# Optimization experiments

Hardware: AMD Instinct MI355X
Metric: run time of the kernel (lower is better)

Reference implementation:

```python
import jax, jax.numpy as jnp
import numpy as np

D, E, FF = 512, 8, 4 * 512
BS, H, W = 2, 32, 32
T = BS * H * W


def setup_inputs() -> dict:
    key = jax.random.key(0)
    ks = jax.random.split(key, 12)
    s = lambda fan_in: 1.0 / np.sqrt(fan_in)
    return {
        "x": jax.random.normal(ks[0], (BS, D, H, W), dtype=jnp.float32),
        "Wg": jax.random.normal(ks[1], (D, E), dtype=jnp.float32) * s(D),
        "bg": jnp.zeros((E,), dtype=jnp.float32),
        "Wn": jax.random.normal(ks[2], (D, E), dtype=jnp.float32) * s(D),
        "bn": jnp.zeros((E,), dtype=jnp.float32),
        "W1": jax.random.normal(ks[3], (E, D, FF), dtype=jnp.float32) * s(D),
        "b1": jnp.zeros((E, FF), dtype=jnp.float32),
        "W2": jax.random.normal(ks[4], (E, FF, D), dtype=jnp.float32) * s(FF),
        "b2": jnp.zeros((E, D), dtype=jnp.float32),
        "noise_eps": jax.random.normal(ks[5], (T, E), dtype=jnp.float32),
        "top_k": 2,
    }


def reference(x, Wg, bg, Wn, bn, W1, b1, W2, b2, noise_eps, top_k):
    bs, d, h, w = x.shape
    tokens = x.transpose(0, 2, 3, 1).reshape(-1, d)  # [T, d]
    t = tokens.shape[0]
    # Noisy top-k router
    logits = tokens @ Wg + bg                                  # [T, E]
    noise = noise_eps * jax.nn.softplus(tokens @ Wn + bn)      # [T, E]
    noisy = logits + noise
    top_v, top_i = jax.lax.top_k(noisy, top_k)                 # [T, k]
    sparse = jnp.full_like(noisy, -jnp.inf)
    sparse = sparse.at[jnp.arange(t)[:, None], top_i].set(top_v)
    gates = jax.nn.softmax(sparse, axis=-1)                    # [T, E], zero off top-k
    # Expert MLPs (dense over experts; gates zero-out non-selected)
    hdn = jax.nn.relu(jnp.einsum("td,edf->tef", tokens, W1) + b1)  # [T, E, 4d]
    out_e = jnp.einsum("tef,efd->ted", hdn, W2) + b2               # [T, E, d]
    out = jnp.einsum("te,ted->td", gates, out_e)                   # combine
    return out.reshape(bs, h, w, d).transpose(0, 3, 1, 2)
```

## Files before the change

### kernel.cpp

```cpp
#include <hip/hip_runtime.h>
#include <hip/hip_bf16.h>
#include <math.h>

#define DD  512
#define EE  8
#define FFD 2048
#define TT  2048
#define HWH 1024

typedef __bf16 b16x8 __attribute__((ext_vector_type(8)));
typedef float  f32x4 __attribute__((ext_vector_type(4)));

__device__ __forceinline__ unsigned short f2bf(float f) {
    unsigned u = __builtin_bit_cast(unsigned, f);
    u = (u + 0x7FFFu + ((u >> 16) & 1u)) >> 16;
    return (unsigned short)u;
}

__device__ __forceinline__ void gload16(const void* g, void* l) {
    __builtin_amdgcn_global_load_lds(
        (const __attribute__((address_space(1))) void*)g,
        (__attribute__((address_space(3))) void*)l, 16, 0, 0);
}

__device__ __forceinline__ int seg_pred(const int* __restrict__ cnt, int e) {
    int s = 0;
    #pragma unroll
    for (int i = 0; i < EE; ++i) s += (i < e) ? cnt[i] : 0;
    return s;
}

__global__ __launch_bounds__(256) void moe_prep(
    const float* __restrict__ W1, const float* __restrict__ W2,
    const float* __restrict__ x,
    unsigned short* __restrict__ W1t, unsigned short* __restrict__ W2t,
    unsigned short* __restrict__ xb,
    const float* __restrict__ Wg, const float* __restrict__ Wn,
    float* __restrict__ part, int* __restrict__ cnt)
{
    __shared__ float ld[128][65];
    int which = blockIdx.z, e = blockIdx.y;
    int tid = threadIdx.x;

    if (which == 3) {
        if (e == 0 && blockIdx.x == 0 && tid < EE) cnt[tid] = 0;
        if (blockIdx.x >= 32) return;
        int u = tid & 63;
        int q = tid >> 6;
        int tt = blockIdx.x, dc = e;
        int t = tt * 64 + u;
        int b = t >> 10, hw = t & 1023;
        const float* xp = x + (size_t)b * DD * HWH + hw;
        int d0 = dc * 64 + q * 16;
        float accL[EE], accN[EE];
        #pragma unroll
        for (int k = 0; k < EE; ++k) { accL[k] = 0.f; accN[k] = 0.f; }
        #pragma unroll
        for (int i = 0; i < 16; ++i) {
            int d = d0 + i;
            float tv = xp[(size_t)d * HWH];
            #pragma unroll
            for (int k = 0; k < EE; ++k) {
                accL[k] = fmaf(tv, Wg[d * EE + k], accL[k]);
                accN[k] = fmaf(tv, Wn[d * EE + k], accN[k]);
            }
        }
        float (*s)[64][16] = (float (*)[64][16])&ld[0][0];
        #pragma unroll
        for (int k = 0; k < EE; ++k) { s[q][u][k] = accL[k]; s[q][u][k + 8] = accN[k]; }
        __syncthreads();
        int idx = tid * 4;
        int ot = idx >> 4, oc = idx & 15;
        float4 v;
        v.x = s[0][ot][oc+0] + s[1][ot][oc+0] + s[2][ot][oc+0] + s[3][ot][oc+0];
        v.y = s[0][ot][oc+1] + s[1][ot][oc+1] + s[2][ot][oc+1] + s[3][ot][oc+1];
        v.z = s[0][ot][oc+2] + s[1][ot][oc+2] + s[2][ot][oc+2] + s[3][ot][oc+2];
        v.w = s[0][ot][oc+3] + s[1][ot][oc+3] + s[2][ot][oc+3] + s[3][ot][oc+3];
        *(float4*)&part[((size_t)dc * TT + tt * 64 + ot) * 16 + oc] = v;
        return;
    }

    const float* in; unsigned short* out; int R, C;
    if (which == 0)      { R = DD;  C = FFD; in = W1 + (size_t)e*DD*FFD; out = W1t + (size_t)e*FFD*DD; }
    else if (which == 1) { R = FFD; C = DD;  in = W2 + (size_t)e*FFD*DD; out = W2t + (size_t)e*DD*FFD; }
    else { if (e >= 2) return; R = DD; C = HWH; in = x + (size_t)e*DD*HWH; out = xb + (size_t)e*HWH*DD; }
    int tilesC = C >> 6, tilesR = R >> 7;
    if ((int)blockIdx.x >= tilesR * tilesC) return;
    int tr = (blockIdx.x / tilesC) << 7, tc = (blockIdx.x % tilesC) << 6;
    int ty = tid >> 4, tx = tid & 15;
    #pragma unroll
    for (int i = 0; i < 8; ++i) {
        int r = ty + i * 16;
        const float4 v = *(const float4*)&in[(size_t)(tr + r)*C + tc + tx*4];
        ld[r][tx*4+0] = v.x; ld[r][tx*4+1] = v.y;
        ld[r][tx*4+2] = v.z; ld[r][tx*4+3] = v.w;
    }
    __syncthreads();
    int ox = tid & 15;
    #pragma unroll
    for (int it = 0; it < 4; ++it) {
        int c = (tid >> 4) + it * 16;
        uint4 u;
        u.x = f2bf(ld[ox*8+0][c]) | ((unsigned)f2bf(ld[ox*8+1][c]) << 16);
        u.y = f2bf(ld[ox*8+2][c]) | ((unsigned)f2bf(ld[ox*8+3][c]) << 16);
        u.z = f2bf(ld[ox*8+4][c]) | ((unsigned)f2bf(ld[ox*8+5][c]) << 16);
        u.w = f2bf(ld[ox*8+6][c]) | ((unsigned)f2bf(ld[ox*8+7][c]) << 16);
        *(uint4*)&out[(size_t)(tc + c)*R + tr + ox*8] = u;
    }
}

__global__ __launch_bounds__(256) void moe_router_topk(
    const float* __restrict__ part,
    const float* __restrict__ bg, const float* __restrict__ bn,
    const float* __restrict__ neps,
    int* __restrict__ cnt, int* __restrict__ pair0, int* __restrict__ pair1,
    int* __restrict__ ltok, float* __restrict__ lgate)
{
    int t = blockIdx.x * 256 + threadIdx.x;
    float L[EE], N[EE];
    #pragma unroll
    for (int e = 0; e < EE; ++e) { L[e] = bg[e]; N[e] = bn[e]; }
    #pragma unroll
    for (int dc = 0; dc < 8; ++dc) {
        const float* p = &part[((size_t)dc * TT + t) * 16];
        float4 a0 = *(const float4*)&p[0];
        float4 a1 = *(const float4*)&p[4];
        float4 a2 = *(const float4*)&p[8];
        float4 a3 = *(const float4*)&p[12];
        L[0] += a0.x; L[1] += a0.y; L[2] += a0.z; L[3] += a0.w;
        L[4] += a1.x; L[5] += a1.y; L[6] += a1.z; L[7] += a1.w;
        N[0] += a2.x; N[1] += a2.y; N[2] += a2.z; N[3] += a2.w;
        N[4] += a3.x; N[5] += a3.y; N[6] += a3.z; N[7] += a3.w;
    }
    float noisy[EE];
    #pragma unroll
    for (int e = 0; e < EE; ++e) {
        float sp = fmaxf(N[e], 0.f) + log1pf(expf(-fabsf(N[e])));
        noisy[e] = L[e] + neps[t * EE + e] * sp;
    }
    int e0 = 0; float v0 = noisy[0];
    #pragma unroll
    for (int e = 1; e < EE; ++e) if (noisy[e] > v0) { v0 = noisy[e]; e0 = e; }
    int e1 = (e0 == 0) ? 1 : 0; float v1 = noisy[e1];
    #pragma unroll
    for (int e = 0; e < EE; ++e)
        if (e != e0 && e != e1 && noisy[e] > v1) { v1 = noisy[e]; e1 = e; }
    float ex  = expf(v1 - v0);
    float inv = 1.f / (1.f + ex);
    float g0 = inv, g1 = ex * inv;
    int p0 = atomicAdd(&cnt[e0], 1);
    int p1 = atomicAdd(&cnt[e1], 1);
    ltok[e0 * TT + p0] = t; lgate[e0 * TT + p0] = g0;
    ltok[e1 * TT + p1] = t; lgate[e1 * TT + p1] = g1;
    pair0[t] = (e0 << 16) | p0;
    pair1[t] = (e1 << 16) | p1;
}

__global__ __launch_bounds__(256, 3) void moe_gemm1(
    const unsigned short* __restrict__ xb, const unsigned short* __restrict__ W1t,
    const float* __restrict__ b1, const int* __restrict__ cnt,
    const int* __restrict__ ltok, unsigned short* __restrict__ Hbuf)
{
    int e = blockIdx.x, mt = blockIdx.y, nt = blockIdx.z;
    int ce = cnt[e];
    if (mt * 64 >= ce) return;
    int s0 = seg_pred(cnt, e);
    const unsigned short* Be = W1t + (size_t)e * FFD * DD;
    __shared__ unsigned short As[2][64 * 64];
    __shared__ unsigned short Bs[2][128 * 64];
    int tid = threadIdx.x, lane = tid & 63, wv = tid >> 6;

    int srow = lane >> 3, schunk = lane & 7;
    int srcoff = ((schunk ^ srow) << 3);

    size_t aoff[2]; int ards[2];
    #pragma unroll
    for (int c = 0; c < 2; ++c) {
        int r0 = (c*4 + wv)*8;
        int ri = mt*64 + r0 + srow;
        int tok = ltok[e * TT + (ri < ce ? ri : 0)];
        aoff[c] = (size_t)tok * DD + srcoff;
        ards[c] = r0 * 64;
    }
    size_t boff[4]; int brds[4];
    #pragma unroll
    for (int c = 0; c < 4; ++c) {
        int r0 = (c*4 + wv)*8;
        boff[c] = (size_t)(nt*128 + r0 + srow) * DD + srcoff;
        brds[c] = r0 * 64;
    }

    int frow = lane & 15, fk = (lane >> 4) * 8;
    int am = (wv >> 1) * 32, bnn = (wv & 1) * 64;
    int rx = (frow & 7) << 3;

    f32x4 acc[2][4];
    f32x4 zero = {0.f, 0.f, 0.f, 0.f};
    #pragma unroll
    for (int m = 0; m < 2; ++m)
        #pragma unroll
        for (int n = 0; n < 4; ++n) acc[m][n] = zero;

    #pragma unroll
    for (int c = 0; c < 2; ++c) gload16(&xb[aoff[c]], &As[0][ards[c]]);
    #pragma unroll
    for (int c = 0; c < 4; ++c) gload16(&Be[boff[c]], &Bs[0][brds[c]]);
    #pragma unroll
    for (int c = 0; c < 2; ++c) gload16(&xb[aoff[c] + 64], &As[1][ards[c]]);
    #pragma unroll
    for (int c = 0; c < 4; ++c) gload16(&Be[boff[c] + 64], &Bs[1][brds[c]]);

    #pragma unroll
    for (int t = 0; t < 8; ++t) {
        if (t < 6) { asm volatile("s_waitcnt vmcnt(6)" ::: "memory"); }
        else       { asm volatile("s_waitcnt vmcnt(0)" ::: "memory"); }
        __builtin_amdgcn_s_barrier();
        __builtin_amdgcn_sched_barrier(0);
        const int cur = t & 1;
        #pragma unroll
        for (int k2 = 0; k2 < 64; k2 += 32) {
            b16x8 af[2], bf[4];
            #pragma unroll
            for (int m = 0; m < 2; ++m)
                af[m] = *(const b16x8*)&As[cur][(am + m*16 + frow)*64 + ((k2 + fk) ^ rx)];
            #pragma unroll
            for (int n = 0; n < 4; ++n)
                bf[n] = *(const b16x8*)&Bs[cur][(bnn + n*16 + frow)*64 + ((k2 + fk) ^ rx)];
            #pragma unroll
            for (int m = 0; m < 2; ++m)
                #pragma unroll
                for (int n = 0; n < 4; ++n)
                    acc[m][n] = __builtin_amdgcn_mfma_f32_16x16x32_bf16(af[m], bf[n], acc[m][n], 0, 0, 0);
        }
        __builtin_amdgcn_s_barrier();
        if (t < 6) {
            int kk = (t + 2) * 64;
            #pragma unroll
            for (int c = 0; c < 2; ++c) gload16(&xb[aoff[c] + kk], &As[cur][ards[c]]);
            #pragma unroll
            for (int c = 0; c < 4; ++c) gload16(&Be[boff[c] + kk], &Bs[cur][brds[c]]);
        }
    }

    int crow = (lane >> 4) * 4;
    #pragma unroll
    for (int m = 0; m < 2; ++m) {
        #pragma unroll
        for (int i = 0; i < 4; ++i) {
            int r = mt*64 + am + m*16 + crow + i;
            if (r < ce) {
                size_t hrow = (size_t)(s0 + r) * FFD;
                #pragma unroll
                for (int n = 0; n < 4; ++n) {
                    int col = nt*128 + bnn + n*16 + frow;
                    float v = acc[m][n][i] + b1[e * FFD + col];
                    Hbuf[hrow + col] = f2bf(fmaxf(v, 0.f));
                }
            }
        }
    }
}

__global__ __launch_bounds__(256, 3) void moe_gemm2(
    const unsigned short* __restrict__ Hbuf, const unsigned short* __restrict__ W2t,
    const int* __restrict__ cnt, float* __restrict__ P2)
{
    int e = blockIdx.x, mt = blockIdx.y;
    int split = blockIdx.z >> 2, nt = blockIdx.z & 3;
    int ce = cnt[e];
    if (mt * 64 >= ce) return;
    int s0 = seg_pred(cnt, e);
    int kbase = split * 1024;
    const unsigned short* Be = W2t + (size_t)e * DD * FFD;
    __shared__ unsigned short As[2][64 * 64];
    __shared__ unsigned short Bs[2][128 * 64];
    int tid = threadIdx.x, lane = tid & 63, wv = tid >> 6;

    int srow = lane >> 3, schunk = lane & 7;
    int srcoff = ((schunk ^ srow) << 3);

    size_t aoff[2]; int ards[2];
    #pragma unroll
    for (int c = 0; c < 2; ++c) {
        int r0 = (c*4 + wv)*8;
        int g = s0 + mt*64 + r0 + srow; if (g > 4095) g = 4095;
        aoff[c] = (size_t)g * FFD + kbase + srcoff;
        ards[c] = r0 * 64;
    }
    size_t boff[4]; int brds[4];
    #pragma unroll
    for (int c = 0; c < 4; ++c) {
        int r0 = (c*4 + wv)*8;
        boff[c] = (size_t)(nt*128 + r0 + srow) * FFD + kbase + srcoff;
        brds[c] = r0 * 64;
    }

    int frow = lane & 15, fk = (lane >> 4) * 8;
    int am = (wv >> 1) * 32, bnn = (wv & 1) * 64;
    int rx = (frow & 7) << 3;

    f32x4 acc[2][4];
    f32x4 zero = {0.f, 0.f, 0.f, 0.f};
    #pragma unroll
    for (int m = 0; m < 2; ++m)
        #pragma unroll
        for (int n = 0; n < 4; ++n) acc[m][n] = zero;

    #pragma unroll
    for (int c = 0; c < 2; ++c) gload16(&Hbuf[aoff[c]], &As[0][ards[c]]);
    #pragma unroll
    for (int c = 0; c < 4; ++c) gload16(&Be[boff[c]], &Bs[0][brds[c]]);
    #pragma unroll
    for (int c = 0; c < 2; ++c) gload16(&Hbuf[aoff[c] + 64], &As[1][ards[c]]);
    #pragma unroll
    for (int c = 0; c < 4; ++c) gload16(&Be[boff[c] + 64], &Bs[1][brds[c]]);

    #pragma unroll
    for (int t = 0; t < 16; ++t) {
        if (t < 14) { asm volatile("s_waitcnt vmcnt(6)" ::: "memory"); }
        else        { asm volatile("s_waitcnt vmcnt(0)" ::: "memory"); }
        __builtin_amdgcn_s_barrier();
        __builtin_amdgcn_sched_barrier(0);
        const int cur = t & 1;
        #pragma unroll
        for (int k2 = 0; k2 < 64; k2 += 32) {
            b16x8 af[2], bf[4];
            #pragma unroll
            for (int m = 0; m < 2; ++m)
                af[m] = *(const b16x8*)&As[cur][(am + m*16 + frow)*64 + ((k2 + fk) ^ rx)];
            #pragma unroll
            for (int n = 0; n < 4; ++n)
                bf[n] = *(const b16x8*)&Bs[cur][(bnn + n*16 + frow)*64 + ((k2 + fk) ^ rx)];
            #pragma unroll
            for (int m = 0; m < 2; ++m)
                #pragma unroll
                for (int n = 0; n < 4; ++n)
                    acc[m][n] = __builtin_amdgcn_mfma_f32_16x16x32_bf16(af[m], bf[n], acc[m][n], 0, 0, 0);
        }
        __builtin_amdgcn_s_barrier();
        if (t < 14) {
            int kk = (t + 2) * 64;
            #pragma unroll
            for (int c = 0; c < 2; ++c) gload16(&Hbuf[aoff[c] + kk], &As[cur][ards[c]]);
            #pragma unroll
            for (int c = 0; c < 4; ++c) gload16(&Be[boff[c] + kk], &Bs[cur][brds[c]]);
        }
    }

    int crow = (lane >> 4) * 4;
    float* Pw = P2 + (size_t)split * 4096 * DD;
    #pragma unroll
    for (int m = 0; m < 2; ++m) {
        #pragma unroll
        for (int i = 0; i < 4; ++i) {
            int r = mt*64 + am + m*16 + crow + i;
            if (r < ce) {
                size_t prow = (size_t)(s0 + r) * DD;
                #pragma unroll
                for (int n = 0; n < 4; ++n) {
                    int col = nt*128 + bnn + n*16 + frow;
                    Pw[prow + col] = acc[m][n][i];
                }
            }
        }
    }
}

__global__ __launch_bounds__(256) void moe_combine(
    const int* __restrict__ pair0, const int* __restrict__ pair1,
    const int* __restrict__ cnt, const float* __restrict__ lgate,
    const float* __restrict__ b2, const float* __restrict__ P2,
    float* __restrict__ out)
{
    __shared__ float tile[32][68];
    int tid = threadIdx.x;
    int ti = blockIdx.x, dc = blockIdx.y;
    int ty = tid >> 3, tx = tid & 7;
    int t = ti * 32 + ty;
    int a0 = pair0[t], a1 = pair1[t];
    int e0 = a0 >> 16, sl0 = a0 & 0xFFFF;
    int e1 = a1 >> 16, sl1 = a1 & 0xFFFF;
    int p0 = seg_pred(cnt, e0) + sl0, p1 = seg_pred(cnt, e1) + sl1;
    float g0 = lgate[e0 * TT + sl0], g1 = lgate[e1 * TT + sl1];
    int d0 = dc * 64 + tx * 8;
    f32x4 s0v[2] = {{0,0,0,0},{0,0,0,0}}, s1v[2] = {{0,0,0,0},{0,0,0,0}};
    #pragma unroll
    for (int s = 0; s < 2; ++s) {
        const f32x4* r0p = (const f32x4*)(P2 + ((size_t)s * 4096 + p0) * DD + d0);
        const f32x4* r1p = (const f32x4*)(P2 + ((size_t)s * 4096 + p1) * DD + d0);
        s0v[0] += r0p[0]; s0v[1] += r0p[1];
        s1v[0] += r1p[0]; s1v[1] += r1p[1];
    }
    const f32x4* b0p = (const f32x4*)(b2 + e0 * DD + d0);
    const f32x4* b1p = (const f32x4*)(b2 + e1 * DD + d0);
    #pragma unroll
    for (int q = 0; q < 2; ++q) {
        f32x4 v = g0 * (s0v[q] + b0p[q]) + g1 * (s1v[q] + b1p[q]);
        *(f32x4*)&tile[ty][tx*8 + q*4] = v;
    }
    __syncthreads();
    int dy = tid >> 2, hx = tid & 3;
    int b = (ti * 32) >> 10, hw0 = (ti * 32) & 1023;
    size_t obase = ((size_t)(b * DD + dc * 64 + dy)) * HWH + hw0;
    #pragma unroll
    for (int q = 0; q < 2; ++q) {
        int j = hx * 8 + q * 4;
        float4 w;
        w.x = tile[j + 0][dy];
        w.y = tile[j + 1][dy];
        w.z = tile[j + 2][dy];
        w.w = tile[j + 3][dy];
        *(float4*)&out[obase + j] = w;
    }
}

extern "C" void kernel_launch(void* const* d_in, const int* in_sizes, int n_in,
                              void* d_out, int out_size, void* d_ws, size_t ws_size,
                              hipStream_t stream)
{
    const float* x    = (const float*)d_in[0];
    const float* Wg   = (const float*)d_in[1];
    const float* bg   = (const float*)d_in[2];
    const float* Wn   = (const float*)d_in[3];
    const float* bn   = (const float*)d_in[4];
    const float* W1   = (const float*)d_in[5];
    const float* b1   = (const float*)d_in[6];
    const float* W2   = (const float*)d_in[7];
    const float* b2   = (const float*)d_in[8];
    const float* neps = (const float*)d_in[9];

    char* ws = (char*)d_ws;
    int*   cnt   = (int*)(ws + 0);
    int*   pair0 = (int*)(ws + 512);
    int*   pair1 = (int*)(ws + 8704);
    int*   ltok  = (int*)(ws + 32768);
    float* lgate = (float*)(ws + 98304);
    float* part  = (float*)(ws + 163840);
    unsigned short* xb   = (unsigned short*)(ws + 1212416);
    unsigned short* Hbuf = (unsigned short*)(ws + 3309568);
    unsigned short* W1t  = (unsigned short*)(ws + 20086784);
    unsigned short* W2t  = (unsigned short*)(ws + 36864000);
    float*          P2   = (float*)(ws + 53641216);

    moe_prep<<<dim3(128, 8, 4), 256, 0, stream>>>(W1, W2, x, W1t, W2t, xb, Wg, Wn, part, cnt);
    moe_router_topk<<<TT / 256, 256, 0, stream>>>(part, bg, bn, neps,
                                                  cnt, pair0, pair1, ltok, lgate);
    moe_gemm1<<<dim3(EE, 32, 16), 256, 0, stream>>>(xb, W1t, b1, cnt, ltok, Hbuf);
    moe_gemm2<<<dim3(EE, 32, 8), 256, 0, stream>>>(Hbuf, W2t, cnt, P2);
    moe_combine<<<dim3(TT / 32, 8), 256, 0, stream>>>(pair0, pair1, cnt, lgate, b2, P2, (float*)d_out);
}
```

Measured before the change: 91.42 us.

## Load A operand fragments directly from global into registers, drop A LDS tile

Both expert GEMM kernels now fetch their activation (A) fragments straight from global memory into double-buffered registers in MFMA fragment layout, instead of staging them through shared memory. The B tile stays in LDS. This frees LDS and removes A-side LDS writes and reads, and the launch bounds are raised from 3 to 4 blocks per CU. In exchange the A loads are narrower per-thread global reads with poorer coalescing, some rows are fetched redundantly by two waves, and register pressure rises. The vmcnt wait thresholds are retuned to account for the extra in-flight loads.

Measured after the change: 134.8 us. +47.4%, slower.

```diff
diff --git a/kernel.cpp b/kernel.cpp
--- a/kernel.cpp
+++ b/kernel.cpp
@@ -156,7 +156,7 @@
     pair1[t] = (e1 << 16) | p1;
 }
 
-__global__ __launch_bounds__(256, 3) void moe_gemm1(
+__global__ __launch_bounds__(256, 4) void moe_gemm1(
     const unsigned short* __restrict__ xb, const unsigned short* __restrict__ W1t,
     const float* __restrict__ b1, const int* __restrict__ cnt,
     const int* __restrict__ ltok, unsigned short* __restrict__ Hbuf)
@@ -166,22 +166,11 @@
     if (mt * 64 >= ce) return;
     int s0 = seg_pred(cnt, e);
     const unsigned short* Be = W1t + (size_t)e * FFD * DD;
-    __shared__ unsigned short As[2][64 * 64];
     __shared__ unsigned short Bs[2][128 * 64];
     int tid = threadIdx.x, lane = tid & 63, wv = tid >> 6;
 
     int srow = lane >> 3, schunk = lane & 7;
     int srcoff = ((schunk ^ srow) << 3);
-
-    size_t aoff[2]; int ards[2];
-    #pragma unroll
-    for (int c = 0; c < 2; ++c) {
-        int r0 = (c*4 + wv)*8;
-        int ri = mt*64 + r0 + srow;
-        int tok = ltok[e * TT + (ri < ce ? ri : 0)];
-        aoff[c] = (size_t)tok * DD + srcoff;
-        ards[c] = r0 * 64;
-    }
     size_t boff[4]; int brds[4];
     #pragma unroll
     for (int c = 0; c < 4; ++c) {
@@ -194,6 +183,10 @@
     int am = (wv >> 1) * 32, bnn = (wv & 1) * 64;
     int rx = (frow & 7) << 3;
 
+    int r0 = mt*64 + am + frow, r1 = r0 + 16;
+    const unsigned short* ap0 = xb + (size_t)ltok[e*TT + (r0 < ce ? r0 : 0)] * DD + fk;
+    const unsigned short* ap1 = xb + (size_t)ltok[e*TT + (r1 < ce ? r1 : 0)] * DD + fk;
+
     f32x4 acc[2][4];
     f32x4 zero = {0.f, 0.f, 0.f, 0.f};
     #pragma unroll
@@ -201,28 +194,31 @@
         #pragma unroll
         for (int n = 0; n < 4; ++n) acc[m][n] = zero;
 
-    #pragma unroll
-    for (int c = 0; c < 2; ++c) gload16(&xb[aoff[c]], &As[0][ards[c]]);
+    b16x8 ra[2][2][2];
+
     #pragma unroll
     for (int c = 0; c < 4; ++c) gload16(&Be[boff[c]], &Bs[0][brds[c]]);
-    #pragma unroll
-    for (int c = 0; c < 2; ++c) gload16(&xb[aoff[c] + 64], &As[1][ards[c]]);
+    __builtin_amdgcn_sched_barrier(0);
+    ra[0][0][0] = *(const b16x8*)&ap0[0];  ra[0][0][1] = *(const b16x8*)&ap0[32];
+    ra[0][1][0] = *(const b16x8*)&ap1[0];  ra[0][1][1] = *(const b16x8*)&ap1[32];
+    __builtin_amdgcn_sched_barrier(0);
     #pragma unroll
     for (int c = 0; c < 4; ++c) gload16(&Be[boff[c] + 64], &Bs[1][brds[c]]);
+    __builtin_amdgcn_sched_barrier(0);
+    ra[1][0][0] = *(const b16x8*)&ap0[64]; ra[1][0][1] = *(const b16x8*)&ap0[96];
+    ra[1][1][0] = *(const b16x8*)&ap1[64]; ra[1][1][1] = *(const b16x8*)&ap1[96];
+    __builtin_amdgcn_sched_barrier(0);
 
     #pragma unroll
     for (int t = 0; t < 8; ++t) {
-        if (t < 6) { asm volatile("s_waitcnt vmcnt(6)" ::: "memory"); }
+        if (t < 7) { asm volatile("s_waitcnt vmcnt(8)" ::: "memory"); }
         else       { asm volatile("s_waitcnt vmcnt(0)" ::: "memory"); }
         __builtin_amdgcn_s_barrier();
         __builtin_amdgcn_sched_barrier(0);
         const int cur = t & 1;
         #pragma unroll
         for (int k2 = 0; k2 < 64; k2 += 32) {
-            b16x8 af[2], bf[4];
-            #pragma unroll
-            for (int m = 0; m < 2; ++m)
-                af[m] = *(const b16x8*)&As[cur][(am + m*16 + frow)*64 + ((k2 + fk) ^ rx)];
+            b16x8 bf[4];
             #pragma unroll
             for (int n = 0; n < 4; ++n)
                 bf[n] = *(const b16x8*)&Bs[cur][(bnn + n*16 + frow)*64 + ((k2 + fk) ^ rx)];
@@ -230,15 +226,17 @@
             for (int m = 0; m < 2; ++m)
                 #pragma unroll
                 for (int n = 0; n < 4; ++n)
-                    acc[m][n] = __builtin_amdgcn_mfma_f32_16x16x32_bf16(af[m], bf[n], acc[m][n], 0, 0, 0);
+                    acc[m][n] = __builtin_amdgcn_mfma_f32_16x16x32_bf16(ra[cur][m][k2 >> 5], bf[n], acc[m][n], 0, 0, 0);
         }
         __builtin_amdgcn_s_barrier();
         if (t < 6) {
             int kk = (t + 2) * 64;
             #pragma unroll
-            for (int c = 0; c < 2; ++c) gload16(&xb[aoff[c] + kk], &As[cur][ards[c]]);
-            #pragma unroll
             for (int c = 0; c < 4; ++c) gload16(&Be[boff[c] + kk], &Bs[cur][brds[c]]);
+            __builtin_amdgcn_sched_barrier(0);
+            ra[cur][0][0] = *(const b16x8*)&ap0[kk];      ra[cur][0][1] = *(const b16x8*)&ap0[kk + 32];
+            ra[cur][1][0] = *(const b16x8*)&ap1[kk];      ra[cur][1][1] = *(const b16x8*)&ap1[kk + 32];
+            __builtin_amdgcn_sched_barrier(0);
         }
     }
 
@@ -261,7 +259,7 @@
     }
 }
 
-__global__ __launch_bounds__(256, 3) void moe_gemm2(
+__global__ __launch_bounds__(256, 4) void moe_gemm2(
     const unsigned short* __restrict__ Hbuf, const unsigned short* __restrict__ W2t,
     const int* __restrict__ cnt, float* __restrict__ P2)
 {
@@ -272,21 +270,11 @@
     int s0 = seg_pred(cnt, e);
     int kbase = split * 1024;
     const unsigned short* Be = W2t + (size_t)e * DD * FFD;
-    __shared__ unsigned short As[2][64 * 64];
     __shared__ unsigned short Bs[2][128 * 64];
     int tid = threadIdx.x, lane = tid & 63, wv = tid >> 6;
 
     int srow = lane >> 3, schunk = lane & 7;
     int srcoff = ((schunk ^ srow) << 3);
-
-    size_t aoff[2]; int ards[2];
-    #pragma unroll
-    for (int c = 0; c < 2; ++c) {
-        int r0 = (c*4 + wv)*8;
-        int g = s0 + mt*64 + r0 + srow; if (g > 4095) g = 4095;
-        aoff[c] = (size_t)g * FFD + kbase + srcoff;
-        ards[c] = r0 * 64;
-    }
     size_t boff[4]; int brds[4];
     #pragma unroll
     for (int c = 0; c < 4; ++c) {
@@ -299,6 +287,11 @@
     int am = (wv >> 1) * 32, bnn = (wv & 1) * 64;
     int rx = (frow & 7) << 3;
 
+    int g0 = s0 + mt*64 + am + frow; if (g0 > 4095) g0 = 4095;
+    int g1 = g0 + 16;                if (g1 > 4095) g1 = 4095;
+    const unsigned short* ap0 = Hbuf + (size_t)g0 * FFD + kbase + fk;
+    const unsigned short* ap1 = Hbuf + (size_t)g1 * FFD + kbase + fk;
+
     f32x4 acc[2][4];
     f32x4 zero = {0.f, 0.f, 0.f, 0.f};
     #pragma unroll
@@ -306,28 +299,31 @@
         #pragma unroll
         for (int n = 0; n < 4; ++n) acc[m][n] = zero;
 
-    #pragma unroll
-    for (int c = 0; c < 2; ++c) gload16(&Hbuf[aoff[c]], &As[0][ards[c]]);
+    b16x8 ra[2][2][2];
+
     #pragma unroll
     for (int c = 0; c < 4; ++c) gload16(&Be[boff[c]], &Bs[0][brds[c]]);
-    #pragma unroll
-    for (int c = 0; c < 2; ++c) gload16(&Hbuf[aoff[c] + 64], &As[1][ards[c]]);
+    __builtin_amdgcn_sched_barrier(0);
+    ra[0][0][0] = *(const b16x8*)&ap0[0];  ra[0][0][1] = *(const b16x8*)&ap0[32];
+    ra[0][1][0] = *(const b16x8*)&ap1[0];  ra[0][1][1] = *(const b16x8*)&ap1[32];
+    __builtin_amdgcn_sched_barrier(0);
     #pragma unroll
     for (int c = 0; c < 4; ++c) gload16(&Be[boff[c] + 64], &Bs[1][brds[c]]);
+    __builtin_amdgcn_sched_barrier(0);
+    ra[1][0][0] = *(const b16x8*)&ap0[64]; ra[1][0][1] = *(const b16x8*)&ap0[96];
+    ra[1][1][0] = *(const b16x8*)&ap1[64]; ra[1][1][1] = *(const b16x8*)&ap1[96];
+    __builtin_amdgcn_sched_barrier(0);
 
     #pragma unroll
     for (int t = 0; t < 16; ++t) {
-        if (t < 14) { asm volatile("s_waitcnt vmcnt(6)" ::: "memory"); }
+        if (t < 15) { asm volatile("s_waitcnt vmcnt(8)" ::: "memory"); }
         else        { asm volatile("s_waitcnt vmcnt(0)" ::: "memory"); }
         __builtin_amdgcn_s_barrier();
         __builtin_amdgcn_sched_barrier(0);
         const int cur = t & 1;
         #pragma unroll
         for (int k2 = 0; k2 < 64; k2 += 32) {
-            b16x8 af[2], bf[4];
-            #pragma unroll
-            for (int m = 0; m < 2; ++m)
-                af[m] = *(const b16x8*)&As[cur][(am + m*16 + frow)*64 + ((k2 + fk) ^ rx)];
+            b16x8 bf[4];
             #pragma unroll
             for (int n = 0; n < 4; ++n)
                 bf[n] = *(const b16x8*)&Bs[cur][(bnn + n*16 + frow)*64 + ((k2 + fk) ^ rx)];
@@ -335,15 +331,17 @@
             for (int m = 0; m < 2; ++m)
                 #pragma unroll
                 for (int n = 0; n < 4; ++n)
-                    acc[m][n] = __builtin_amdgcn_mfma_f32_16x16x32_bf16(af[m], bf[n], acc[m][n], 0, 0, 0);
+                    acc[m][n] = __builtin_amdgcn_mfma_f32_16x16x32_bf16(ra[cur][m][k2 >> 5], bf[n], acc[m][n], 0, 0, 0);
         }
         __builtin_amdgcn_s_barrier();
         if (t < 14) {
             int kk = (t + 2) * 64;
             #pragma unroll
-            for (int c = 0; c < 2; ++c) gload16(&Hbuf[aoff[c] + kk], &As[cur][ards[c]]);
-            #pragma unroll
             for (int c = 0; c < 4; ++c) gload16(&Be[boff[c] + kk], &Bs[cur][brds[c]]);
+            __builtin_amdgcn_sched_barrier(0);
+            ra[cur][0][0] = *(const b16x8*)&ap0[kk];      ra[cur][0][1] = *(const b16x8*)&ap0[kk + 32];
+            ra[cur][1][0] = *(const b16x8*)&ap1[kk];      ra[cur][1][1] = *(const b16x8*)&ap1[kk + 32];
+            __builtin_amdgcn_sched_barrier(0);
         }
     }
 
```

## Enlarge gemm1 M-tile to 128 and fold gate and bias into gemm2 epilogue

Applied to the files above, without the earlier changes.

Doubles the token-row tile of the first expert GEMM from 64 to 128 rows per block. Each block now does four rows of MFMA fragments per wave, so each W1 tile loaded from memory is reused across more tokens. Gate scaling and the b2 bias move from the combine kernel into the gemm2 epilogue, with bias added only by split 0, so combine just sums four partial rows. The s_waitcnt thresholds are relaxed on the second-to-last iteration to overlap more loads. In exchange there are more accumulator registers, lower occupancy (launch bounds 2), and fewer gemm1 blocks.

After: 99.97 us. +9.4%, slower.

```diff
diff --git a/kernel.cpp b/kernel.cpp
--- a/kernel.cpp
+++ b/kernel.cpp
@@ -156,28 +156,28 @@
     pair1[t] = (e1 << 16) | p1;
 }
 
-__global__ __launch_bounds__(256, 3) void moe_gemm1(
+__global__ __launch_bounds__(256, 2) void moe_gemm1(
     const unsigned short* __restrict__ xb, const unsigned short* __restrict__ W1t,
     const float* __restrict__ b1, const int* __restrict__ cnt,
     const int* __restrict__ ltok, unsigned short* __restrict__ Hbuf)
 {
     int e = blockIdx.x, mt = blockIdx.y, nt = blockIdx.z;
     int ce = cnt[e];
-    if (mt * 64 >= ce) return;
+    if (mt * 128 >= ce) return;
     int s0 = seg_pred(cnt, e);
     const unsigned short* Be = W1t + (size_t)e * FFD * DD;
-    __shared__ unsigned short As[2][64 * 64];
+    __shared__ unsigned short As[2][128 * 64];
     __shared__ unsigned short Bs[2][128 * 64];
     int tid = threadIdx.x, lane = tid & 63, wv = tid >> 6;
 
     int srow = lane >> 3, schunk = lane & 7;
     int srcoff = ((schunk ^ srow) << 3);
 
-    size_t aoff[2]; int ards[2];
-    #pragma unroll
-    for (int c = 0; c < 2; ++c) {
+    size_t aoff[4]; int ards[4];
+    #pragma unroll
+    for (int c = 0; c < 4; ++c) {
         int r0 = (c*4 + wv)*8;
-        int ri = mt*64 + r0 + srow;
+        int ri = mt*128 + r0 + srow;
         int tok = ltok[e * TT + (ri < ce ? ri : 0)];
         aoff[c] = (size_t)tok * DD + srcoff;
         ards[c] = r0 * 64;
@@ -191,43 +191,43 @@
     }
 
     int frow = lane & 15, fk = (lane >> 4) * 8;
-    int am = (wv >> 1) * 32, bnn = (wv & 1) * 64;
+    int am = (wv >> 1) * 64, bnn = (wv & 1) * 64;
     int rx = (frow & 7) << 3;
 
-    f32x4 acc[2][4];
+    f32x4 acc[4][4];
     f32x4 zero = {0.f, 0.f, 0.f, 0.f};
     #pragma unroll
-    for (int m = 0; m < 2; ++m)
+    for (int m = 0; m < 4; ++m)
         #pragma unroll
         for (int n = 0; n < 4; ++n) acc[m][n] = zero;
 
     #pragma unroll
-    for (int c = 0; c < 2; ++c) gload16(&xb[aoff[c]], &As[0][ards[c]]);
+    for (int c = 0; c < 4; ++c) gload16(&xb[aoff[c]], &As[0][ards[c]]);
     #pragma unroll
     for (int c = 0; c < 4; ++c) gload16(&Be[boff[c]], &Bs[0][brds[c]]);
     #pragma unroll
-    for (int c = 0; c < 2; ++c) gload16(&xb[aoff[c] + 64], &As[1][ards[c]]);
+    for (int c = 0; c < 4; ++c) gload16(&xb[aoff[c] + 64], &As[1][ards[c]]);
     #pragma unroll
     for (int c = 0; c < 4; ++c) gload16(&Be[boff[c] + 64], &Bs[1][brds[c]]);
 
     #pragma unroll
     for (int t = 0; t < 8; ++t) {
-        if (t < 6) { asm volatile("s_waitcnt vmcnt(6)" ::: "memory"); }
+        if (t < 7) { asm volatile("s_waitcnt vmcnt(8)" ::: "memory"); }
         else       { asm volatile("s_waitcnt vmcnt(0)" ::: "memory"); }
         __builtin_amdgcn_s_barrier();
         __builtin_amdgcn_sched_barrier(0);
         const int cur = t & 1;
         #pragma unroll
         for (int k2 = 0; k2 < 64; k2 += 32) {
-            b16x8 af[2], bf[4];
-            #pragma unroll
-            for (int m = 0; m < 2; ++m)
+            b16x8 af[4], bf[4];
+            #pragma unroll
+            for (int m = 0; m < 4; ++m)
                 af[m] = *(const b16x8*)&As[cur][(am + m*16 + frow)*64 + ((k2 + fk) ^ rx)];
             #pragma unroll
             for (int n = 0; n < 4; ++n)
                 bf[n] = *(const b16x8*)&Bs[cur][(bnn + n*16 + frow)*64 + ((k2 + fk) ^ rx)];
             #pragma unroll
-            for (int m = 0; m < 2; ++m)
+            for (int m = 0; m < 4; ++m)
                 #pragma unroll
                 for (int n = 0; n < 4; ++n)
                     acc[m][n] = __builtin_amdgcn_mfma_f32_16x16x32_bf16(af[m], bf[n], acc[m][n], 0, 0, 0);
@@ -236,7 +236,7 @@
         if (t < 6) {
             int kk = (t + 2) * 64;
             #pragma unroll
-            for (int c = 0; c < 2; ++c) gload16(&xb[aoff[c] + kk], &As[cur][ards[c]]);
+            for (int c = 0; c < 4; ++c) gload16(&xb[aoff[c] + kk], &As[cur][ards[c]]);
             #pragma unroll
             for (int c = 0; c < 4; ++c) gload16(&Be[boff[c] + kk], &Bs[cur][brds[c]]);
         }
@@ -244,10 +244,10 @@
 
     int crow = (lane >> 4) * 4;
     #pragma unroll
-    for (int m = 0; m < 2; ++m) {
+    for (int m = 0; m < 4; ++m) {
         #pragma unroll
         for (int i = 0; i < 4; ++i) {
-            int r = mt*64 + am + m*16 + crow + i;
+            int r = mt*128 + am + m*16 + crow + i;
             if (r < ce) {
                 size_t hrow = (size_t)(s0 + r) * FFD;
                 #pragma unroll
@@ -263,7 +263,8 @@
 
 __global__ __launch_bounds__(256, 3) void moe_gemm2(
     const unsigned short* __restrict__ Hbuf, const unsigned short* __restrict__ W2t,
-    const int* __restrict__ cnt, float* __restrict__ P2)
+    const float* __restrict__ b2, const int* __restrict__ cnt,
+    const float* __restrict__ lgate, float* __restrict__ P2)
 {
     int e = blockIdx.x, mt = blockIdx.y;
     int split = blockIdx.z >> 2, nt = blockIdx.z & 3;
@@ -317,7 +318,7 @@
 
     #pragma unroll
     for (int t = 0; t < 16; ++t) {
-        if (t < 14) { asm volatile("s_waitcnt vmcnt(6)" ::: "memory"); }
+        if (t < 15) { asm volatile("s_waitcnt vmcnt(6)" ::: "memory"); }
         else        { asm volatile("s_waitcnt vmcnt(0)" ::: "memory"); }
         __builtin_amdgcn_s_barrier();
         __builtin_amdgcn_sched_barrier(0);
@@ -355,11 +356,14 @@
         for (int i = 0; i < 4; ++i) {
             int r = mt*64 + am + m*16 + crow + i;
             if (r < ce) {
+                float g = lgate[e * TT + r];
                 size_t prow = (size_t)(s0 + r) * DD;
                 #pragma unroll
                 for (int n = 0; n < 4; ++n) {
                     int col = nt*128 + bnn + n*16 + frow;
-                    Pw[prow + col] = acc[m][n][i];
+                    float v = acc[m][n][i];
+                    if (split == 0) v += b2[e * DD + col];
+                    Pw[prow + col] = g * v;
                 }
             }
         }
@@ -368,8 +372,7 @@
 
 __global__ __launch_bounds__(256) void moe_combine(
     const int* __restrict__ pair0, const int* __restrict__ pair1,
-    const int* __restrict__ cnt, const float* __restrict__ lgate,
-    const float* __restrict__ b2, const float* __restrict__ P2,
+    const int* __restrict__ cnt, const float* __restrict__ P2,
     float* __restrict__ out)
 {
     __shared__ float tile[32][68];
@@ -378,24 +381,16 @@
     int ty = tid >> 3, tx = tid & 7;
     int t = ti * 32 + ty;
     int a0 = pair0[t], a1 = pair1[t];
-    int e0 = a0 >> 16, sl0 = a0 & 0xFFFF;
-    int e1 = a1 >> 16, sl1 = a1 & 0xFFFF;
-    int p0 = seg_pred(cnt, e0) + sl0, p1 = seg_pred(cnt, e1) + sl1;
-    float g0 = lgate[e0 * TT + sl0], g1 = lgate[e1 * TT + sl1];
+    int p0 = seg_pred(cnt, a0 >> 16) + (a0 & 0xFFFF);
+    int p1 = seg_pred(cnt, a1 >> 16) + (a1 & 0xFFFF);
     int d0 = dc * 64 + tx * 8;
-    f32x4 s0v[2] = {{0,0,0,0},{0,0,0,0}}, s1v[2] = {{0,0,0,0},{0,0,0,0}};
-    #pragma unroll
-    for (int s = 0; s < 2; ++s) {
-        const f32x4* r0p = (const f32x4*)(P2 + ((size_t)s * 4096 + p0) * DD + d0);
-        const f32x4* r1p = (const f32x4*)(P2 + ((size_t)s * 4096 + p1) * DD + d0);
-        s0v[0] += r0p[0]; s0v[1] += r0p[1];
-        s1v[0] += r1p[0]; s1v[1] += r1p[1];
-    }
-    const f32x4* b0p = (const f32x4*)(b2 + e0 * DD + d0);
-    const f32x4* b1p = (const f32x4*)(b2 + e1 * DD + d0);
+    const f32x4* r00 = (const f32x4*)(P2 + (size_t)p0 * DD + d0);
+    const f32x4* r01 = (const f32x4*)(P2 + ((size_t)4096 + p0) * DD + d0);
+    const f32x4* r10 = (const f32x4*)(P2 + (size_t)p1 * DD + d0);
+    const f32x4* r11 = (const f32x4*)(P2 + ((size_t)4096 + p1) * DD + d0);
     #pragma unroll
     for (int q = 0; q < 2; ++q) {
-        f32x4 v = g0 * (s0v[q] + b0p[q]) + g1 * (s1v[q] + b1p[q]);
+        f32x4 v = (r00[q] + r01[q]) + (r10[q] + r11[q]);
         *(f32x4*)&tile[ty][tx*8 + q*4] = v;
     }
     __syncthreads();
@@ -445,7 +440,7 @@
     moe_prep<<<dim3(128, 8, 4), 256, 0, stream>>>(W1, W2, x, W1t, W2t, xb, Wg, Wn, part, cnt);
     moe_router_topk<<<TT / 256, 256, 0, stream>>>(part, bg, bn, neps,
                                                   cnt, pair0, pair1, ltok, lgate);
-    moe_gemm1<<<dim3(EE, 32, 16), 256, 0, stream>>>(xb, W1t, b1, cnt, ltok, Hbuf);
-    moe_gemm2<<<dim3(EE, 32, 8), 256, 0, stream>>>(Hbuf, W2t, cnt, P2);
-    moe_combine<<<dim3(TT / 32, 8), 256, 0, stream>>>(pair0, pair1, cnt, lgate, b2, P2, (float*)d_out);
-}
+    moe_gemm1<<<dim3(EE, 16, 16), 256, 0, stream>>>(xb, W1t, b1, cnt, ltok, Hbuf);
+    moe_gemm2<<<dim3(EE, 32, 8), 256, 0, stream>>>(Hbuf, W2t, b2, cnt, lgate, P2);
+    moe_combine<<<dim3(TT / 32, 8), 256, 0, stream>>>(pair0, pair1, cnt, P2, (float*)d_out);
+}
```
